# Optimization experiments

Measured on AMD Instinct MI355X. Metric: run time of the kernel, lower is better.

## Reference

```python
import jax, jax.numpy as jnp
import numpy as np

B, NODES, D, DEG = 256, 124, 32, 16
N = B * NODES
EP = NODES * DEG
E = B * EP
L, H, C = 3, 4, 32
NCLS = 40
TMP = 124 + 32 * 2 * L
EPS = 1e-5
NEG_SLOPE = 0.2


def setup_inputs() -> dict:
    key = jax.random.key(0)
    ks = jax.random.split(key, 16)
    x = jax.random.normal(ks[0], (N, D), dtype=jnp.float32)
    # per-graph random edges, guaranteed no self-loops
    src = jax.random.randint(ks[1], (B, EP), 0, NODES)
    off = jax.random.randint(ks[2], (B, EP), 1, NODES)
    dst = (src + off) % NODES
    goff = (jnp.arange(B) * NODES)[:, None]
    edge_index = jnp.stack([(src + goff).reshape(-1), (dst + goff).reshape(-1)]).astype(jnp.int32)
    batch = jnp.repeat(jnp.arange(B), NODES).astype(jnp.int32)
    conv_W = jax.random.normal(ks[3], (L, D, H * C), dtype=jnp.float32) / np.sqrt(D)
    conv_att_l = jax.random.normal(ks[4], (L, H, C), dtype=jnp.float32) * 0.1
    conv_att_r = jax.random.normal(ks[5], (L, H, C), dtype=jnp.float32) * 0.1
    conv_bias = jnp.zeros((L, C), dtype=jnp.float32)
    bn_gamma = jnp.ones((L, C), dtype=jnp.float32)
    bn_beta = jnp.zeros((L, C), dtype=jnp.float32)
    lin1_W = jax.random.normal(ks[6], (NODES * C, 124), dtype=jnp.float32) / np.sqrt(NODES * C)
    lin1_b = jnp.zeros((124,), dtype=jnp.float32)
    bn1_gamma = jnp.ones((124,), dtype=jnp.float32)
    bn1_beta = jnp.zeros((124,), dtype=jnp.float32)
    lin2_W = jax.random.normal(ks[7], (TMP, NCLS), dtype=jnp.float32) / np.sqrt(TMP)
    lin2_b = jnp.zeros((NCLS,), dtype=jnp.float32)
    return dict(x=x, edge_index=edge_index, batch=batch, conv_W=conv_W,
                conv_att_l=conv_att_l, conv_att_r=conv_att_r, conv_bias=conv_bias,
                bn_gamma=bn_gamma, bn_beta=bn_beta, lin1_W=lin1_W, lin1_b=lin1_b,
                bn1_gamma=bn1_gamma, bn1_beta=bn1_beta, lin2_W=lin2_W, lin2_b=lin2_b)


def _supergat_mx(x, src, dst, W, att_l, att_r, bias):
    # SuperGATConv, attention_type='MX', concat=False (mean over heads), eval mode
    h = (x @ W).reshape(N, H, C)              # [N,H,C]
    x_j = h[src]                              # source / message features [E',H,C]
    x_i = h[dst]                              # target features
    logits = jnp.sum(x_i * x_j, -1)           # [E',H] dot-product logits
    alpha = jnp.sum(x_j * att_l, -1) + jnp.sum(x_i * att_r, -1)
    alpha = alpha * jax.nn.sigmoid(logits)
    alpha = jax.nn.leaky_relu(alpha, NEG_SLOPE)
    # scatter-softmax over incoming edges of each target node
    amax = jax.ops.segment_max(alpha, dst, num_segments=N)
    ex = jnp.exp(alpha - amax[dst])
    denom = jax.ops.segment_sum(ex, dst, num_segments=N)
    a = ex / (denom[dst] + 1e-16)             # [E',H]
    out = jax.ops.segment_sum(x_j * a[..., None], dst, num_segments=N)  # [N,H,C]
    return out.mean(axis=1) + bias            # concat=False -> head mean, [N,C]


def _batchnorm(x, gamma, beta):
    mu = x.mean(0)
    var = x.var(0)
    return (x - mu) * jax.lax.rsqrt(var + EPS) * gamma + beta


def reference(x, edge_index, batch, conv_W, conv_att_l, conv_att_r, conv_bias,
              bn_gamma, bn_beta, lin1_W, lin1_b, bn1_gamma, bn1_beta, lin2_W, lin2_b):
    # add self loops once (input edges contain none)
    sl = jnp.arange(N, dtype=edge_index.dtype)
    src = jnp.concatenate([edge_index[0], sl])
    dst = jnp.concatenate([edge_index[1], sl])
    inter = []
    for l in range(L):
        x = _supergat_mx(x, src, dst, conv_W[l], conv_att_l[l], conv_att_r[l], conv_bias[l])
        x = _batchnorm(x, bn_gamma[l], bn_beta[l])
        x = jax.nn.relu(x)
        cnt = jax.ops.segment_sum(jnp.ones((N,), x.dtype), batch, num_segments=B)
        gmean = jax.ops.segment_sum(x, batch, num_segments=B) / cnt[:, None]
        gmax = jax.ops.segment_max(x, batch, num_segments=B)
        inter.append(jnp.concatenate([gmean, gmax], 1))   # [B, 2C]
    x = x.reshape(B, NODES * C)
    x = x @ lin1_W + lin1_b
    x = _batchnorm(x, bn1_gamma, bn1_beta)
    x = jnp.concatenate([x] + inter, 1)                   # inter_connect=True
    x = jax.nn.relu(x)
    return x @ lin2_W + lin2_b                            # [B, NCLS]
```

## Files before the change

### kernel.cpp

```cpp
#include <hip/hip_runtime.h>
#include <math.h>

#define NN 31744
#define NE 507904
#define EP 1984
#define NODES 124
#define NB 256
#define CC 32
#define HC 128
#define FEAT_DIM 316
#define NCLS 40
#define NC 3968
#define EXCAP 192

typedef __attribute__((ext_vector_type(8))) short bf16x8;
typedef __attribute__((ext_vector_type(4))) float f32x4;

#define LOG2E  1.44269504f
#define LOG2E5 0.28853901f

__device__ __forceinline__ unsigned short f2bf(float f) {
    unsigned u = __float_as_uint(f);
    u = u + 0x7FFFu + ((u >> 16) & 1u);
    return (unsigned short)(u >> 16);
}
__device__ __forceinline__ float bf2f(unsigned short s) {
    return __uint_as_float(((unsigned)s) << 16);
}

__global__ __launch_bounds__(256) void prep_k(const int* __restrict__ ei,
                                              unsigned* __restrict__ gmask,
                                              int* __restrict__ gdst,
                                              int* __restrict__ gdent,
                                              float* __restrict__ bnacc,
                                              const float* __restrict__ W1,
                                              unsigned short* __restrict__ WT) {
    int t = threadIdx.x;
    if (blockIdx.x >= NB) {
        __shared__ float tile[32][33];
        int bb = blockIdx.x - NB;
        int kb = bb >> 2, jb = bb & 3;
        int tr = t >> 5, tc = t & 31;
        for (int r = tr; r < 32; r += 8) {
            int k = kb * 32 + r, j = jb * 32 + tc;
            tile[r][tc] = (j < 124) ? W1[k * 124 + j] : 0.f;
        }
        __syncthreads();
        for (int r = tr; r < 32; r += 8) {
            int j = jb * 32 + r, k = kb * 32 + tc;
            WT[(size_t)j * NC + k] = f2bf(tile[tc][r]);
        }
        return;
    }
    __shared__ unsigned mcnt[NODES * NODES];
    __shared__ int cnt[128], pref[128];
    __shared__ int locs[124][8];
    int g = blockIdx.x;
    if (g == 0 && t < 192) bnacc[t] = 0.f;
    for (int i = t; i < NODES * NODES; i += 256) mcnt[i] = 0u;
    __syncthreads();
    for (int e = t; e < EP; e += 256) {
        int s = ei[g * EP + e] - g * NODES;
        int d = ei[NE + g * EP + e] - g * NODES;
        atomicAdd(&mcnt[d * NODES + s], 1u);
    }
    __syncthreads();
    int nd = 0;
    if (t < 124) {
        unsigned m[4] = {0u, 0u, 0u, 0u};
        for (int s = 0; s < NODES; ++s) {
            unsigned c = mcnt[t * NODES + s] + (s == t ? 1u : 0u);
            if (c) {
                m[s >> 5] |= 1u << (s & 31);
                if (c > 1u && nd < 8) { locs[t][nd] = (s << 8) | (int)c; nd++; }
            }
        }
        uint4 mm; mm.x = m[0]; mm.y = m[1]; mm.z = m[2]; mm.w = m[3];
        *(uint4*)&gmask[(size_t)(g * NODES + t) * 4] = mm;
        cnt[t] = nd;
    } else if (t < 128) cnt[t] = 0;
    __syncthreads();
    if (t < 128) pref[t] = cnt[t];
    __syncthreads();
    for (int off = 1; off < 128; off <<= 1) {
        int v = (t >= off && t < 128) ? pref[t - off] : 0;
        __syncthreads();
        if (t < 128) pref[t] += v;
        __syncthreads();
    }
    if (t < 124) {
        int off = pref[t] - cnt[t];
        gdst[g * 132 + t] = off < EXCAP ? off : EXCAP;
        for (int j = 0; j < nd; ++j)
            if (off + j < EXCAP) gdent[g * EXCAP + off + j] = locs[t][j];
    }
    if (t == 0) {
        int tot = pref[127];
        gdst[g * 132 + 124] = tot < EXCAP ? tot : EXCAP;
    }
}

#define HS 136
#define TS 136
#define XS 40
#define ABS 136
#define PWS 40

__global__ __launch_bounds__(1024, 1) void conv_graph(
    const float* __restrict__ xin, const float* __restrict__ W,
    const float* __restrict__ attl, const float* __restrict__ attr,
    const float* __restrict__ bias,
    const unsigned* __restrict__ gmask, const int* __restrict__ gdst,
    const int* __restrict__ gdent,
    const float* __restrict__ bnprev, const float* __restrict__ gprev,
    const float* __restrict__ bprev, float* __restrict__ feat, int lprev,
    float* __restrict__ y, float* __restrict__ bnacc) {

    __shared__ short hbh[128 * HS];
    __shared__ short hbl[128 * HS];
    __shared__ short hTall[128 * TS];
    __shared__ short pwbuf[16 * 1280];
    __shared__ short attBuf[16 * ABS];
    __shared__ float ALs[4][128], ARs[4][128];
    __shared__ unsigned mask[128][4];
    __shared__ unsigned short dupst[136];
    __shared__ unsigned dupent[EXCAP];
    __shared__ float bias_s[32];
    __shared__ float bsum[8][32], bsq[8][32];
    __shared__ float pmean[32];
    __shared__ int pmax[32];

    int g = blockIdx.x, t = threadIdx.x, base = g * NODES;
    short* xh  = pwbuf;
    short* xl  = pwbuf + 5120;
    short* WTh = hTall;
    short* WTl = hTall + 5120;

    if (t < 32) { pmean[t] = 0.f; pmax[t] = 0; }
    __syncthreads();

    {
        const float4* xsrc = (const float4*)(xin + (size_t)base * CC);
        for (int i = t; i < 992; i += 1024) {
            float4 v = xsrc[i];
            int n = i >> 3, c4 = i & 7;
            if (lprev >= 0) {
                float vv[4] = {v.x, v.y, v.z, v.w};
#pragma unroll
                for (int q = 0; q < 4; ++q) {
                    int c = c4 * 4 + q;
                    float mu = bnprev[c] * (1.f / NN);
                    float var = bnprev[32 + c] * (1.f / NN) - mu * mu;
                    float sc = rsqrtf(var + 1e-5f) * gprev[c];
                    float xv = (vv[q] - mu) * sc + bprev[c];
                    xv = fmaxf(xv, 0.f);
                    vv[q] = xv;
                    atomicAdd(&pmean[c], xv);
                    atomicMax(&pmax[c], __float_as_int(xv));
                }
                v.x = vv[0]; v.y = vv[1]; v.z = vv[2]; v.w = vv[3];
            }
            unsigned short h0 = f2bf(v.x), h1 = f2bf(v.y), h2 = f2bf(v.z), h3 = f2bf(v.w);
            unsigned short l0 = f2bf(v.x - bf2f(h0)), l1 = f2bf(v.y - bf2f(h1));
            unsigned short l2 = f2bf(v.z - bf2f(h2)), l3 = f2bf(v.w - bf2f(h3));
            uint2 ph; ph.x = ((unsigned)h1 << 16) | h0; ph.y = ((unsigned)h3 << 16) | h2;
            uint2 pl; pl.x = ((unsigned)l1 << 16) | l0; pl.y = ((unsigned)l3 << 16) | l2;
            *(uint2*)&xh[n * XS + c4 * 4] = ph;
            *(uint2*)&xl[n * XS + c4 * 4] = pl;
        }
        if (t < 4 * XS) { xh[124 * XS + t] = 0; xl[124 * XS + t] = 0; }
    }
    {
        int hc = t & 127, mq = t >> 7, ks = mq * 4;
        unsigned short hh4[4], ll4[4];
#pragma unroll
        for (int q = 0; q < 4; ++q) {
            float w = W[(ks + q) * HC + hc];
            hh4[q] = f2bf(w);
            ll4[q] = f2bf(w - bf2f(hh4[q]));
        }
        uint2 ph; ph.x = ((unsigned)hh4[1] << 16) | hh4[0]; ph.y = ((unsigned)hh4[3] << 16) | hh4[2];
        uint2 pl; pl.x = ((unsigned)ll4[1] << 16) | ll4[0]; pl.y = ((unsigned)ll4[3] << 16) | ll4[2];
        *(uint2*)&WTh[hc * XS + ks] = ph;
        *(uint2*)&WTl[hc * XS + ks] = pl;
    }
    for (int i = t; i < 2048; i += 1024) {
        int n = i >> 7, k = i & 127;
        float v = 0.f;
        int hidx = n & 3;
        if (n < 8 && (k >> 5) == hidx)
            v = (n < 4) ? attl[hidx * 32 + (k & 31)] : attr[hidx * 32 + (k & 31)];
        attBuf[n * ABS + k] = (short)f2bf(v);
    }
    if (t < CC) bias_s[t] = bias[t];
    if (t < 128) {
        if (t < 124) {
            uint4 m = *(const uint4*)&gmask[(size_t)(base + t) * 4];
            mask[t][0] = m.x; mask[t][1] = m.y; mask[t][2] = m.z; mask[t][3] = m.w;
        } else { mask[t][0] = 0u; mask[t][1] = 0u; mask[t][2] = 0u; mask[t][3] = 0u; }
    }
    if (t < 136) dupst[t] = (unsigned short)gdst[g * 132 + (t < 124 ? t : 124)];
    if (t >= 832 && t < 832 + EXCAP) dupent[t - 832] = (unsigned)gdent[g * EXCAP + (t - 832)];
    __syncthreads();

    if (lprev >= 0 && t < 32) {
        float* fp = feat + g * FEAT_DIM + NODES + lprev * 64;
        fp[t] = pmean[t] * (1.f / NODES);
        fp[32 + t] = __int_as_float(pmax[t]);
    }

    int wv = t >> 6, l = t & 63;
    int l15 = l & 15, l4 = l >> 4;

#pragma unroll
    for (int j = 0; j < 4; ++j) {
        int idx = wv * 4 + j;
        int tr = idx >> 3, tc = idx & 7;
        bf16x8 ah = *(bf16x8*)&xh[(tr * 16 + l15) * XS + l4 * 8];
        bf16x8 al_ = *(bf16x8*)&xl[(tr * 16 + l15) * XS + l4 * 8];
        bf16x8 bh = *(bf16x8*)&WTh[(tc * 16 + l15) * XS + l4 * 8];
        bf16x8 bl_ = *(bf16x8*)&WTl[(tc * 16 + l15) * XS + l4 * 8];
        f32x4 z = {0.f, 0.f, 0.f, 0.f};
        f32x4 c0 = __builtin_amdgcn_mfma_f32_16x16x32_bf16(ah, bh, z, 0, 0, 0);
        f32x4 c1 = __builtin_amdgcn_mfma_f32_16x16x32_bf16(ah, bl_, z, 0, 0, 0);
        f32x4 c2 = __builtin_amdgcn_mfma_f32_16x16x32_bf16(al_, bh, z, 0, 0, 0);
        f32x4 c = (c0 + c1) + c2;
        int hc = tc * 16 + l15;
#pragma unroll
        for (int r = 0; r < 4; ++r) {
            int n = tr * 16 + l4 * 4 + r;
            float s = c[r];
            unsigned short hi = f2bf(s);
            hbh[n * HS + hc] = (short)hi;
            hbl[n * HS + hc] = (short)f2bf(s - bf2f(hi));
        }
    }
    __syncthreads();

    if (wv < 8) {
        f32x4 c = {0.f, 0.f, 0.f, 0.f};
#pragma unroll
        for (int kb = 0; kb < 4; ++kb) {
            bf16x8 a = *(bf16x8*)&hbh[(wv * 16 + l15) * HS + kb * 32 + l4 * 8];
            bf16x8 b = *(bf16x8*)&attBuf[l15 * ABS + kb * 32 + l4 * 8];
            c = __builtin_amdgcn_mfma_f32_16x16x32_bf16(a, b, c, 0, 0, 0);
        }
        if (l15 < 8) {
#pragma unroll
            for (int r = 0; r < 4; ++r) {
                int n = wv * 16 + l4 * 4 + r;
                if (l15 < 4) ALs[l15][n] = c[r];
                else         ARs[l15 - 4][n] = c[r];
            }
        }
    }
#pragma unroll
    for (int hh2 = 0; hh2 < 4; ++hh2) {
        int k = t & 31, n4 = t >> 5;
        unsigned short r4[4];
#pragma unroll
        for (int r = 0; r < 4; ++r)
            r4[r] = (unsigned short)hbh[(n4 * 4 + r) * HS + hh2 * 32 + k];
        uint2 pk;
        pk.x = ((unsigned)r4[1] << 16) | r4[0];
        pk.y = ((unsigned)r4[3] << 16) | r4[2];
        *(uint2*)&hTall[(hh2 * 32 + k) * TS + n4 * 4] = pk;
    }
    __syncthreads();

    int DJ = wv >> 1;
    float accA[4] = {0.f, 0.f, 0.f, 0.f};
    float accB[4] = {0.f, 0.f, 0.f, 0.f};
    {
        int hh0 = (wv & 1) * 2;
        short* pwb = pwbuf + wv * 1280;
        int dst = DJ * 16 + l15;
        uint4 mrow = *(uint4*)&mask[dst][0];
        unsigned mwords[4] = {mrow.x, mrow.y, mrow.z, mrow.w};
        unsigned cntp[8];
#pragma unroll
        for (int SI = 0; SI < 8; ++SI) {
            unsigned mw = (mwords[SI >> 1] >> ((SI & 1) * 16 + l4 * 4)) & 0xFu;
            cntp[SI] = (mw & 1u) | ((mw & 2u) << 7) | ((mw & 4u) << 14) | ((mw & 8u) << 21);
        }
        {
            int s0 = dupst[dst], s1 = dupst[dst + 1];
            for (int e = s0; e < s1; ++e) {
                unsigned ent = dupent[e];
                unsigned src = (ent >> 8) & 255u;
                unsigned SI = src >> 4;
                unsigned r = (src & 15u) - (unsigned)(l4 * 4);
                if (r < 4u) {
                    unsigned sh = 8u * r;
                    cntp[SI] = (cntp[SI] & ~(255u << sh)) | ((ent & 255u) << sh);
                }
            }
        }

#define GRAM(kb, slot) { \
    _Pragma("unroll") \
    for (int s2 = 0; s2 < 2; ++s2) { \
        int SI = (kb) * 2 + s2; \
        int ao = (SI * 16 + l15) * HS + hh * 32 + l4 * 8; \
        bf16x8 ah = *(bf16x8*)&hbh[ao]; \
        bf16x8 al_ = *(bf16x8*)&hbl[ao]; \
        f32x4 z2 = {0.f, 0.f, 0.f, 0.f}; \
        f32x4 c0 = __builtin_amdgcn_mfma_f32_16x16x32_bf16(ah, gb, z2, 0, 0, 0); \
        f32x4 c1 = __builtin_amdgcn_mfma_f32_16x16x32_bf16(ah, gl, z2, 0, 0, 0); \
        f32x4 c2 = __builtin_amdgcn_mfma_f32_16x16x32_bf16(al_, gb, z2, 0, 0, 0); \
        f32x4 c = (c0 + c1) + c2; \
        int src0 = SI * 16 + l4 * 4; \
        float4 al4 = *(float4*)&ALs[hh][src0]; \
        unsigned cp = cntp[SI]; \
        float pv[4]; \
        _Pragma("unroll") \
        for (int r = 0; r < 4; ++r) { \
            float e2 = __builtin_amdgcn_exp2f(-LOG2E * c[r]); \
            float sig = __builtin_amdgcn_rcpf(1.f + e2); \
            float a2 = (((const float*)&al4)[r] + ar) * sig; \
            float m = fmaxf(a2 * LOG2E, a2 * LOG2E5); \
            float cr = (float)((cp >> (8 * r)) & 255u); \
            pv[r] = __builtin_amdgcn_exp2f(m) * cr; \
        } \
        sden += (pv[0] + pv[1]) + (pv[2] + pv[3]); \
        unsigned w0_, w1_; \
        asm("v_cvt_pk_bf16_f32 %0, %1, %2" : "=v"(w0_) : "v"(pv[0]), "v"(pv[1])); \
        asm("v_cvt_pk_bf16_f32 %0, %1, %2" : "=v"(w1_) : "v"(pv[2]), "v"(pv[3])); \
        uint2 pk_; pk_.x = w0_; pk_.y = w1_; \
        *(uint2*)&pwb[(slot) * 640 + l15 * PWS + s2 * 16 + l4 * 4] = pk_; \
    } }

#define PVOP(kb, slot) { \
    bf16x8 a = *(bf16x8*)&pwb[(slot) * 640 + l15 * PWS + l4 * 8]; \
    bf16x8 b0 = *(bf16x8*)&hTall[(hh * 32 + l15) * TS + (kb) * 32 + l4 * 8]; \
    bf16x8 b1 = *(bf16x8*)&hTall[(hh * 32 + 16 + l15) * TS + (kb) * 32 + l4 * 8]; \
    num0 = __builtin_amdgcn_mfma_f32_16x16x32_bf16(a, b0, num0, 0, 0, 0); \
    num1 = __builtin_amdgcn_mfma_f32_16x16x32_bf16(a, b1, num1, 0, 0, 0); }

#pragma unroll
        for (int jj = 0; jj < 2; ++jj) {
            int hh = hh0 + jj;
            bf16x8 gb = *(bf16x8*)&hbh[dst * HS + hh * 32 + l4 * 8];
            bf16x8 gl = *(bf16x8*)&hbl[dst * HS + hh * 32 + l4 * 8];
            float ar = ARs[hh][dst];
            float sden = 0.f;
            f32x4 num0 = {0.f, 0.f, 0.f, 0.f};
            f32x4 num1 = {0.f, 0.f, 0.f, 0.f};
            GRAM(0, 0);
            GRAM(1, 1); PVOP(0, 0);
            GRAM(2, 0); PVOP(1, 1);
            GRAM(3, 1); PVOP(2, 0);
            PVOP(3, 1);
            sden += __shfl_xor(sden, 16, 64);
            sden += __shfl_xor(sden, 32, 64);
#pragma unroll
            for (int r = 0; r < 4; ++r) {
                float dn = __shfl(sden, l4 * 4 + r, 64) + 1e-16f;
                accA[r] += ((float*)&num0)[r] / dn;
                accB[r] += ((float*)&num1)[r] / dn;
            }
        }
#undef GRAM
#undef PVOP
    }
    __syncthreads();

    float* exch = (float*)pwbuf;
    if (wv & 1) {
#pragma unroll
        for (int r = 0; r < 4; ++r) {
            exch[DJ * 512 + l15 * 16 + l4 * 4 + r] = accA[r];
            exch[DJ * 512 + 256 + l15 * 16 + l4 * 4 + r] = accB[r];
        }
    }
    __syncthreads();

    if (!(wv & 1)) {
        float sA = 0.f, qA = 0.f, sB = 0.f, qB = 0.f;
#pragma unroll
        for (int r = 0; r < 4; ++r) {
            int n = DJ * 16 + l4 * 4 + r;
            float a = accA[r] + exch[DJ * 512 + l15 * 16 + l4 * 4 + r];
            float b = accB[r] + exch[DJ * 512 + 256 + l15 * 16 + l4 * 4 + r];
            a = 0.25f * a + bias_s[l15];
            b = 0.25f * b + bias_s[16 + l15];
            if (n < NODES) {
                y[(size_t)(base + n) * CC + l15] = a;
                y[(size_t)(base + n) * CC + 16 + l15] = b;
                sA += a; qA += a * a; sB += b; qB += b * b;
            }
        }
        sA += __shfl_xor(sA, 16, 64); sA += __shfl_xor(sA, 32, 64);
        qA += __shfl_xor(qA, 16, 64); qA += __shfl_xor(qA, 32, 64);
        sB += __shfl_xor(sB, 16, 64); sB += __shfl_xor(sB, 32, 64);
        qB += __shfl_xor(qB, 16, 64); qB += __shfl_xor(qB, 32, 64);
        if (l < 16) {
            bsum[DJ][l15] = sA; bsum[DJ][16 + l15] = sB;
            bsq[DJ][l15] = qA;  bsq[DJ][16 + l15] = qB;
        }
    }
    __syncthreads();
    if (t < CC) {
        float S = 0.f, Q = 0.f;
#pragma unroll
        for (int w = 0; w < 8; ++w) { S += bsum[w][t]; Q += bsq[w][t]; }
        atomicAdd(&bnacc[t], S);
        atomicAdd(&bnacc[CC + t], Q);
    }
}

__global__ void bn_relu_pool(const float* __restrict__ y, const float* __restrict__ acc,
                             const float* __restrict__ gamma, const float* __restrict__ beta,
                             unsigned short* __restrict__ xbf, float* __restrict__ feat, int l) {
    int g = blockIdx.x;
    int t = threadIdx.x;
    int c = t & 31, r0 = t >> 5;
    float mu = acc[c] * (1.f / NN);
    float var = acc[32 + c] * (1.f / NN) - mu * mu;
    float sc = rsqrtf(var + 1e-5f) * gamma[c];
    float bt = beta[c];
    float s = 0.f, mx = -INFINITY;
    for (int r = r0; r < NODES; r += 4) {
        int i = (g * NODES + r) * CC + c;
        float v = (y[i] - mu) * sc + bt;
        v = fmaxf(v, 0.f);
        xbf[i] = f2bf(v);
        s += v; mx = fmaxf(mx, v);
    }
    __shared__ float ls[128], lm[128];
    ls[t] = s; lm[t] = mx;
    __syncthreads();
    if (t < 32) {
        float S = ls[t] + ls[32 + t] + ls[64 + t] + ls[96 + t];
        float M = fmaxf(fmaxf(lm[t], lm[32 + t]), fmaxf(lm[64 + t], lm[96 + t]));
        float* fp = feat + g * FEAT_DIM + NODES + l * 64;
        fp[t] = S * (1.f / NODES);
        fp[32 + t] = M;
    }
}

#define L1_KS 4
#define L1_KC 992
#define XP 1000
__global__ __launch_bounds__(512) void lin1_mfma(const unsigned short* __restrict__ Xb,
                                                 const unsigned short* __restrict__ WT,
                                                 float* __restrict__ part) {
    __shared__ unsigned short Xs[16 * XP];
    int mt = blockIdx.x >> 2, kp = blockIdx.x & 3;
    int t = threadIdx.x;
    int wv = t >> 6, l = t & 63, l15 = l & 15, l4 = l >> 4;
    int M0 = mt * 16, k0 = kp * L1_KC;
    for (int i = t; i < 16 * 124; i += 512) {
        int r = i / 124, c = i - r * 124;
        *(uint4*)&Xs[r * XP + c * 8] = *(const uint4*)&Xb[(size_t)(M0 + r) * NC + k0 + c * 8];
    }
    __syncthreads();
    int N0 = wv * 16;
    f32x4 acc = {0.f, 0.f, 0.f, 0.f};
#pragma unroll 4
    for (int kk = 0; kk < 31; ++kk) {
        bf16x8 a = *(bf16x8*)&Xs[l15 * XP + kk * 32 + l4 * 8];
        bf16x8 b = *(const bf16x8*)&WT[(size_t)(N0 + l15) * NC + k0 + kk * 32 + l4 * 8];
        acc = __builtin_amdgcn_mfma_f32_16x16x32_bf16(a, b, acc, 0, 0, 0);
    }
    if (N0 + l15 < 124) {
#pragma unroll
        for (int r = 0; r < 4; ++r)
            part[(size_t)kp * NB * 124 + (M0 + l4 * 4 + r) * 124 + N0 + l15] = acc[r];
    }
}

__global__ __launch_bounds__(512) void bn1_fused(const float* __restrict__ part,
                                                 const float* __restrict__ b,
                                                 const float* __restrict__ gamma,
                                                 const float* __restrict__ beta,
                                                 float* __restrict__ out1,
                                                 float* __restrict__ feat) {
    __shared__ float ps[4][124], pq[4][124], smu[124], ssc[124], sbt[124];
    int t = threadIdx.x;
    int c = t & 127, seg = t >> 7;
    float s = 0.f, q = 0.f;
    if (c < 124) {
        float bb = b[c];
        for (int r = seg * 64; r < seg * 64 + 64; ++r) {
            int i = r * 124 + c;
            float v = bb + part[i] + part[NB * 124 + i]
                    + part[2 * NB * 124 + i] + part[3 * NB * 124 + i];
            out1[i] = v;
            s += v; q += v * v;
        }
        ps[seg][c] = s; pq[seg][c] = q;
    }
    __syncthreads();
    if (t < 124) {
        float S = ps[0][t] + ps[1][t] + ps[2][t] + ps[3][t];
        float Q = pq[0][t] + pq[1][t] + pq[2][t] + pq[3][t];
        float mu = S * (1.f / NB);
        float var = Q * (1.f / NB) - mu * mu;
        smu[t] = mu; ssc[t] = rsqrtf(var + 1e-5f) * gamma[t]; sbt[t] = beta[t];
    }
    __syncthreads();
    if (c < 124) {
        for (int r = seg * 64; r < seg * 64 + 64; ++r) {
            float v = (out1[r * 124 + c] - smu[c]) * ssc[c] + sbt[c];
            feat[r * FEAT_DIM + c] = fmaxf(v, 0.f);
        }
    }
}

__global__ void lin2_k(const float* __restrict__ feat, const float* __restrict__ W,
                       const float* __restrict__ b, float* __restrict__ out) {
    __shared__ float psum[8][40];
    int g = blockIdx.x;
    int t = threadIdx.x;
    int j = t % 40, u = t / 40;
    if (u < 8) {
        int k0 = u * 40, k1 = (u == 7) ? FEAT_DIM : k0 + 40;
        float s = 0.f;
        for (int k = k0; k < k1; ++k) s += feat[g * FEAT_DIM + k] * W[k * NCLS + j];
        psum[u][j] = s;
    }
    __syncthreads();
    if (t < NCLS) {
        float s = b[t];
#pragma unroll
        for (int u2 = 0; u2 < 8; ++u2) s += psum[u2][t];
        out[g * NCLS + t] = s;
    }
}

extern "C" void kernel_launch(void* const* d_in, const int* in_sizes, int n_in,
                              void* d_out, int out_size, void* d_ws, size_t ws_size,
                              hipStream_t stream) {
    const float* x      = (const float*)d_in[0];
    const int*   ei     = (const int*)d_in[1];
    const float* conv_W = (const float*)d_in[3];
    const float* att_l  = (const float*)d_in[4];
    const float* att_r  = (const float*)d_in[5];
    const float* conv_b = (const float*)d_in[6];
    const float* bn_g   = (const float*)d_in[7];
    const float* bn_b   = (const float*)d_in[8];
    const float* lin1_W = (const float*)d_in[9];
    const float* lin1_b = (const float*)d_in[10];
    const float* bn1_g  = (const float*)d_in[11];
    const float* bn1_b  = (const float*)d_in[12];
    const float* lin2_W = (const float*)d_in[13];
    const float* lin2_b = (const float*)d_in[14];

    float* ws = (float*)d_ws;
    float* y = ws;
    unsigned short* xbf = (unsigned short*)(y + (size_t)NN * CC);
    float* bnacc = (float*)(xbf + (size_t)NN * CC);
    float* feat  = bnacc + 192;
    float* out1  = feat + NB * FEAT_DIM;
    float* part  = out1 + NB * 124;
    unsigned short* WT = (unsigned short*)(part + L1_KS * NB * 124);
    unsigned* gmask = (unsigned*)(WT + (size_t)128 * NC);
    int* gdst  = (int*)(gmask + (size_t)NN * 4);
    int* gdent = gdst + NB * 132;

    prep_k<<<NB + (NC / 32) * 4, 256, 0, stream>>>(ei, gmask, gdst, gdent, bnacc,
                                                   lin1_W, WT);

    const float* xin = x;
    for (int l = 0; l < 3; ++l) {
        const float* bnprev = (l == 0) ? nullptr : bnacc + (l - 1) * 64;
        const float* gprev  = (l == 0) ? bn_g : bn_g + (l - 1) * CC;
        const float* bprev  = (l == 0) ? bn_b : bn_b + (l - 1) * CC;
        conv_graph<<<NB, 1024, 0, stream>>>(xin, conv_W + l * CC * HC,
                                            att_l + l * HC, att_r + l * HC,
                                            conv_b + l * CC, gmask, gdst, gdent,
                                            bnprev, gprev, bprev, feat, l - 1,
                                            y, bnacc + l * 64);
        xin = y;
    }

    bn_relu_pool<<<NB, 128, 0, stream>>>(y, bnacc + 128, bn_g + 2 * CC, bn_b + 2 * CC,
                                         xbf, feat, 2);
    lin1_mfma<<<64, 512, 0, stream>>>(xbf, WT, part);
    bn1_fused<<<1, 512, 0, stream>>>(part, lin1_b, bn1_g, bn1_b, out1, feat);
    lin2_k<<<NB, 320, 0, stream>>>(feat, lin2_W, lin2_b, (float*)d_out);
}
```

Baseline: 151.3 us.

## Fuse graph adjacency build into first conv and final BN/pool into lin1

The per-graph edge-count/mask/duplicate-list construction moves from prep_k into the first conv_graph launch, which builds it in shared memory and also writes it to global for later layers; prep_k now only transposes lin1 weights and zeroes accumulators and feature slots. The separate bn_relu_pool kernel is removed: lin1_mfma reads fp32 conv output, applies the last batchnorm+ReLU while staging its bf16 tile, and accumulates mean/max pooling into feat with atomics. This drops a launch and the bf16 intermediate round-trip, but adds serial adjacency work to the first conv's critical path and atomic pooling in lin1.

```diff
diff --git a/kernel.cpp b/kernel.cpp
--- a/kernel.cpp
+++ b/kernel.cpp
@@ -28,75 +28,29 @@
     return __uint_as_float(((unsigned)s) << 16);
 }
 
-__global__ __launch_bounds__(256) void prep_k(const int* __restrict__ ei,
-                                              unsigned* __restrict__ gmask,
-                                              int* __restrict__ gdst,
-                                              int* __restrict__ gdent,
+__global__ __launch_bounds__(256) void prep_k(const float* __restrict__ W1,
+                                              unsigned short* __restrict__ WT,
                                               float* __restrict__ bnacc,
-                                              const float* __restrict__ W1,
-                                              unsigned short* __restrict__ WT) {
+                                              float* __restrict__ feat) {
     int t = threadIdx.x;
-    if (blockIdx.x >= NB) {
-        __shared__ float tile[32][33];
-        int bb = blockIdx.x - NB;
-        int kb = bb >> 2, jb = bb & 3;
-        int tr = t >> 5, tc = t & 31;
-        for (int r = tr; r < 32; r += 8) {
-            int k = kb * 32 + r, j = jb * 32 + tc;
-            tile[r][tc] = (j < 124) ? W1[k * 124 + j] : 0.f;
-        }
-        __syncthreads();
-        for (int r = tr; r < 32; r += 8) {
-            int j = jb * 32 + r, k = kb * 32 + tc;
-            WT[(size_t)j * NC + k] = f2bf(tile[tc][r]);
-        }
+    if (blockIdx.x >= 496) {
+        int idx = (blockIdx.x - 496) * 256 + t;
+        int g2 = idx >> 6, slot = idx & 63;
+        feat[g2 * FEAT_DIM + 252 + slot] = 0.f;
         return;
     }
-    __shared__ unsigned mcnt[NODES * NODES];
-    __shared__ int cnt[128], pref[128];
-    __shared__ int locs[124][8];
-    int g = blockIdx.x;
-    if (g == 0 && t < 192) bnacc[t] = 0.f;
-    for (int i = t; i < NODES * NODES; i += 256) mcnt[i] = 0u;
-    __syncthreads();
-    for (int e = t; e < EP; e += 256) {
-        int s = ei[g * EP + e] - g * NODES;
-        int d = ei[NE + g * EP + e] - g * NODES;
-        atomicAdd(&mcnt[d * NODES + s], 1u);
-    }
-    __syncthreads();
-    int nd = 0;
-    if (t < 124) {
-        unsigned m[4] = {0u, 0u, 0u, 0u};
-        for (int s = 0; s < NODES; ++s) {
-            unsigned c = mcnt[t * NODES + s] + (s == t ? 1u : 0u);
-            if (c) {
-                m[s >> 5] |= 1u << (s & 31);
-                if (c > 1u && nd < 8) { locs[t][nd] = (s << 8) | (int)c; nd++; }
-            }
-        }
-        uint4 mm; mm.x = m[0]; mm.y = m[1]; mm.z = m[2]; mm.w = m[3];
-        *(uint4*)&gmask[(size_t)(g * NODES + t) * 4] = mm;
-        cnt[t] = nd;
-    } else if (t < 128) cnt[t] = 0;
-    __syncthreads();
-    if (t < 128) pref[t] = cnt[t];
-    __syncthreads();
-    for (int off = 1; off < 128; off <<= 1) {
-        int v = (t >= off && t < 128) ? pref[t - off] : 0;
-        __syncthreads();
-        if (t < 128) pref[t] += v;
-        __syncthreads();
-    }
-    if (t < 124) {
-        int off = pref[t] - cnt[t];
-        gdst[g * 132 + t] = off < EXCAP ? off : EXCAP;
-        for (int j = 0; j < nd; ++j)
-            if (off + j < EXCAP) gdent[g * EXCAP + off + j] = locs[t][j];
-    }
-    if (t == 0) {
-        int tot = pref[127];
-        gdst[g * 132 + 124] = tot < EXCAP ? tot : EXCAP;
+    __shared__ float tile[32][33];
+    if (blockIdx.x == 0 && t < 192) bnacc[t] = 0.f;
+    int kb = blockIdx.x >> 2, jb = blockIdx.x & 3;
+    int tr = t >> 5, tc = t & 31;
+    for (int r = tr; r < 32; r += 8) {
+        int k = kb * 32 + r, j = jb * 32 + tc;
+        tile[r][tc] = (j < 124) ? W1[k * 124 + j] : 0.f;
+    }
+    __syncthreads();
+    for (int r = tr; r < 32; r += 8) {
+        int j = jb * 32 + r, k = kb * 32 + tc;
+        WT[(size_t)j * NC + k] = f2bf(tile[tc][r]);
     }
 }
 
@@ -110,14 +64,13 @@
     const float* __restrict__ xin, const float* __restrict__ W,
     const float* __restrict__ attl, const float* __restrict__ attr,
     const float* __restrict__ bias,
-    const unsigned* __restrict__ gmask, const int* __restrict__ gdst,
-    const int* __restrict__ gdent,
+    unsigned* __restrict__ gmask, int* __restrict__ gdst, int* __restrict__ gdent,
+    const int* __restrict__ ei,
     const float* __restrict__ bnprev, const float* __restrict__ gprev,
     const float* __restrict__ bprev, float* __restrict__ feat, int lprev,
     float* __restrict__ y, float* __restrict__ bnacc) {
 
-    __shared__ short hbh[128 * HS];
-    __shared__ short hbl[128 * HS];
+    __shared__ short hpool[2 * 128 * HS];
     __shared__ short hTall[128 * TS];
     __shared__ short pwbuf[16 * 1280];
     __shared__ short attBuf[16 * ABS];
@@ -129,7 +82,10 @@
     __shared__ float bsum[8][32], bsq[8][32];
     __shared__ float pmean[32];
     __shared__ int pmax[32];
-
+    __shared__ int cnt_s[128], pref_s[128];
+
+    short* hbh = hpool;
+    short* hbl = hpool + 128 * HS;
     int g = blockIdx.x, t = threadIdx.x, base = g * NODES;
     short* xh  = pwbuf;
     short* xl  = pwbuf + 5120;
@@ -170,20 +126,6 @@
         }
         if (t < 4 * XS) { xh[124 * XS + t] = 0; xl[124 * XS + t] = 0; }
     }
-    {
-        int hc = t & 127, mq = t >> 7, ks = mq * 4;
-        unsigned short hh4[4], ll4[4];
-#pragma unroll
-        for (int q = 0; q < 4; ++q) {
-            float w = W[(ks + q) * HC + hc];
-            hh4[q] = f2bf(w);
-            ll4[q] = f2bf(w - bf2f(hh4[q]));
-        }
-        uint2 ph; ph.x = ((unsigned)hh4[1] << 16) | hh4[0]; ph.y = ((unsigned)hh4[3] << 16) | hh4[2];
-        uint2 pl; pl.x = ((unsigned)ll4[1] << 16) | ll4[0]; pl.y = ((unsigned)ll4[3] << 16) | ll4[2];
-        *(uint2*)&WTh[hc * XS + ks] = ph;
-        *(uint2*)&WTl[hc * XS + ks] = pl;
-    }
     for (int i = t; i < 2048; i += 1024) {
         int n = i >> 7, k = i & 127;
         float v = 0.f;
@@ -193,21 +135,94 @@
         attBuf[n * ABS + k] = (short)f2bf(v);
     }
     if (t < CC) bias_s[t] = bias[t];
-    if (t < 128) {
+
+    if (lprev < 0) {
+        unsigned* mcnt = (unsigned*)hpool;
+        int (*locs)[8] = (int(*)[8])hTall;
+        for (int i = t; i < NODES * NODES; i += 1024) mcnt[i] = 0u;
+        __syncthreads();
+        for (int e = t; e < EP; e += 1024) {
+            int s = ei[g * EP + e] - base;
+            int d = ei[NE + g * EP + e] - base;
+            atomicAdd(&mcnt[d * NODES + s], 1u);
+        }
+        __syncthreads();
+        int nd = 0;
         if (t < 124) {
-            uint4 m = *(const uint4*)&gmask[(size_t)(base + t) * 4];
-            mask[t][0] = m.x; mask[t][1] = m.y; mask[t][2] = m.z; mask[t][3] = m.w;
-        } else { mask[t][0] = 0u; mask[t][1] = 0u; mask[t][2] = 0u; mask[t][3] = 0u; }
-    }
-    if (t < 136) dupst[t] = (unsigned short)gdst[g * 132 + (t < 124 ? t : 124)];
-    if (t >= 832 && t < 832 + EXCAP) dupent[t - 832] = (unsigned)gdent[g * EXCAP + (t - 832)];
-    __syncthreads();
-
+            unsigned m[4] = {0u, 0u, 0u, 0u};
+            for (int s = 0; s < NODES; ++s) {
+                unsigned c = mcnt[t * NODES + s] + (s == t ? 1u : 0u);
+                if (c) {
+                    m[s >> 5] |= 1u << (s & 31);
+                    if (c > 1u && nd < 8) { locs[t][nd] = (s << 8) | (int)c; nd++; }
+                }
+            }
+            mask[t][0] = m[0]; mask[t][1] = m[1]; mask[t][2] = m[2]; mask[t][3] = m[3];
+            uint4 mm; mm.x = m[0]; mm.y = m[1]; mm.z = m[2]; mm.w = m[3];
+            *(uint4*)&gmask[(size_t)(base + t) * 4] = mm;
+            cnt_s[t] = nd;
+        } else if (t < 128) {
+            cnt_s[t] = 0;
+            mask[t][0] = 0u; mask[t][1] = 0u; mask[t][2] = 0u; mask[t][3] = 0u;
+        }
+        __syncthreads();
+        if (t < 128) pref_s[t] = cnt_s[t];
+        __syncthreads();
+        for (int off = 1; off < 128; off <<= 1) {
+            int v = (t >= off && t < 128) ? pref_s[t - off] : 0;
+            __syncthreads();
+            if (t < 128) pref_s[t] += v;
+            __syncthreads();
+        }
+        if (t < 124) {
+            int off = pref_s[t] - cnt_s[t];
+            int offc = off < EXCAP ? off : EXCAP;
+            dupst[t] = (unsigned short)offc;
+            gdst[g * 132 + t] = offc;
+            for (int j = 0; j < nd; ++j)
+                if (off + j < EXCAP) {
+                    dupent[off + j] = (unsigned)locs[t][j];
+                    gdent[g * EXCAP + off + j] = locs[t][j];
+                }
+        } else if (t < 136) {
+            int tot = pref_s[127];
+            int totc = tot < EXCAP ? tot : EXCAP;
+            dupst[t] = (unsigned short)totc;
+            if (t == 124) gdst[g * 132 + 124] = totc;
+        }
+        __syncthreads();
+    } else {
+        if (t < 128) {
+            if (t < 124) {
+                uint4 m = *(const uint4*)&gmask[(size_t)(base + t) * 4];
+                mask[t][0] = m.x; mask[t][1] = m.y; mask[t][2] = m.z; mask[t][3] = m.w;
+            } else { mask[t][0] = 0u; mask[t][1] = 0u; mask[t][2] = 0u; mask[t][3] = 0u; }
+        }
+        if (t < 136) dupst[t] = (unsigned short)gdst[g * 132 + (t < 124 ? t : 124)];
+        if (t >= 832 && t < 832 + EXCAP) dupent[t - 832] = (unsigned)gdent[g * EXCAP + (t - 832)];
+        __syncthreads();
+    }
+
+    {
+        int hc = t & 127, mq = t >> 7, ks = mq * 4;
+        unsigned short hh4[4], ll4[4];
+#pragma unroll
+        for (int q = 0; q < 4; ++q) {
+            float w = W[(ks + q) * HC + hc];
+            hh4[q] = f2bf(w);
+            ll4[q] = f2bf(w - bf2f(hh4[q]));
+        }
+        uint2 ph; ph.x = ((unsigned)hh4[1] << 16) | hh4[0]; ph.y = ((unsigned)hh4[3] << 16) | hh4[2];
+        uint2 pl; pl.x = ((unsigned)ll4[1] << 16) | ll4[0]; pl.y = ((unsigned)ll4[3] << 16) | ll4[2];
+        *(uint2*)&WTh[hc * XS + ks] = ph;
+        *(uint2*)&WTl[hc * XS + ks] = pl;
+    }
     if (lprev >= 0 && t < 32) {
         float* fp = feat + g * FEAT_DIM + NODES + lprev * 64;
         fp[t] = pmean[t] * (1.f / NODES);
         fp[32 + t] = __int_as_float(pmax[t]);
     }
+    __syncthreads();
 
     int wv = t >> 6, l = t & 63;
     int l15 = l & 15, l4 = l >> 4;
@@ -409,52 +424,59 @@
     }
 }
 
-__global__ void bn_relu_pool(const float* __restrict__ y, const float* __restrict__ acc,
-                             const float* __restrict__ gamma, const float* __restrict__ beta,
-                             unsigned short* __restrict__ xbf, float* __restrict__ feat, int l) {
-    int g = blockIdx.x;
-    int t = threadIdx.x;
-    int c = t & 31, r0 = t >> 5;
-    float mu = acc[c] * (1.f / NN);
-    float var = acc[32 + c] * (1.f / NN) - mu * mu;
-    float sc = rsqrtf(var + 1e-5f) * gamma[c];
-    float bt = beta[c];
-    float s = 0.f, mx = -INFINITY;
-    for (int r = r0; r < NODES; r += 4) {
-        int i = (g * NODES + r) * CC + c;
-        float v = (y[i] - mu) * sc + bt;
-        v = fmaxf(v, 0.f);
-        xbf[i] = f2bf(v);
-        s += v; mx = fmaxf(mx, v);
-    }
-    __shared__ float ls[128], lm[128];
-    ls[t] = s; lm[t] = mx;
-    __syncthreads();
-    if (t < 32) {
-        float S = ls[t] + ls[32 + t] + ls[64 + t] + ls[96 + t];
-        float M = fmaxf(fmaxf(lm[t], lm[32 + t]), fmaxf(lm[64 + t], lm[96 + t]));
-        float* fp = feat + g * FEAT_DIM + NODES + l * 64;
-        fp[t] = S * (1.f / NODES);
-        fp[32 + t] = M;
-    }
-}
-
 #define L1_KS 4
 #define L1_KC 992
 #define XP 1000
-__global__ __launch_bounds__(512) void lin1_mfma(const unsigned short* __restrict__ Xb,
+__global__ __launch_bounds__(512) void lin1_mfma(const float* __restrict__ Y,
+                                                 const float* __restrict__ bnacc,
+                                                 const float* __restrict__ bng,
+                                                 const float* __restrict__ bnb,
                                                  const unsigned short* __restrict__ WT,
-                                                 float* __restrict__ part) {
+                                                 float* __restrict__ part,
+                                                 float* __restrict__ feat) {
     __shared__ unsigned short Xs[16 * XP];
+    __shared__ float smu[32], ssc[32], sbt[32];
     int mt = blockIdx.x >> 2, kp = blockIdx.x & 3;
     int t = threadIdx.x;
+    if (t < 32) {
+        float mu = bnacc[128 + t] * (1.f / NN);
+        float var = bnacc[160 + t] * (1.f / NN) - mu * mu;
+        smu[t] = mu;
+        ssc[t] = rsqrtf(var + 1e-5f) * bng[2 * CC + t];
+        sbt[t] = bnb[2 * CC + t];
+    }
+    __syncthreads();
+    int M0 = mt * 16, k0 = kp * L1_KC;
+    for (int i = t; i < 16 * 248; i += 512) {
+        int r = i / 248, c4 = i - r * 248;
+        float4 v = *(const float4*)&Y[(size_t)(M0 + r) * NC + k0 + c4 * 4];
+        int cb = (c4 * 4) & 31;
+        float vv[4] = {v.x, v.y, v.z, v.w};
+        unsigned short hb[4];
+#pragma unroll
+        for (int q = 0; q < 4; ++q) {
+            int c = cb + q;
+            float xv = fmaxf((vv[q] - smu[c]) * ssc[c] + sbt[c], 0.f);
+            hb[q] = f2bf(xv);
+        }
+        uint2 pk;
+        pk.x = ((unsigned)hb[1] << 16) | hb[0];
+        pk.y = ((unsigned)hb[3] << 16) | hb[2];
+        *(uint2*)&Xs[r * XP + c4 * 4] = pk;
+    }
+    __syncthreads();
+    {
+        int gl = t >> 5, ch = t & 31;
+        float s = 0.f, mx = 0.f;
+        for (int nd2 = 0; nd2 < 31; ++nd2) {
+            float v = bf2f(Xs[gl * XP + nd2 * 32 + ch]);
+            s += v; mx = fmaxf(mx, v);
+        }
+        float* fp = feat + (size_t)(M0 + gl) * FEAT_DIM + 252;
+        atomicAdd(&fp[ch], s * (1.f / NODES));
+        atomicMax((int*)&fp[32 + ch], __float_as_int(mx));
+    }
     int wv = t >> 6, l = t & 63, l15 = l & 15, l4 = l >> 4;
-    int M0 = mt * 16, k0 = kp * L1_KC;
-    for (int i = t; i < 16 * 124; i += 512) {
-        int r = i / 124, c = i - r * 124;
-        *(uint4*)&Xs[r * XP + c * 8] = *(const uint4*)&Xb[(size_t)(M0 + r) * NC + k0 + c * 8];
-    }
-    __syncthreads();
     int N0 = wv * 16;
     f32x4 acc = {0.f, 0.f, 0.f, 0.f};
 #pragma unroll 4
@@ -549,8 +571,7 @@
 
     float* ws = (float*)d_ws;
     float* y = ws;
-    unsigned short* xbf = (unsigned short*)(y + (size_t)NN * CC);
-    float* bnacc = (float*)(xbf + (size_t)NN * CC);
+    float* bnacc = y + (size_t)NN * CC;
     float* feat  = bnacc + 192;
     float* out1  = feat + NB * FEAT_DIM;
     float* part  = out1 + NB * 124;
@@ -559,8 +580,7 @@
     int* gdst  = (int*)(gmask + (size_t)NN * 4);
     int* gdent = gdst + NB * 132;
 
-    prep_k<<<NB + (NC / 32) * 4, 256, 0, stream>>>(ei, gmask, gdst, gdent, bnacc,
-                                                   lin1_W, WT);
+    prep_k<<<560, 256, 0, stream>>>(lin1_W, WT, bnacc, feat);
 
     const float* xin = x;
     for (int l = 0; l < 3; ++l) {
@@ -569,15 +589,13 @@
         const float* bprev  = (l == 0) ? bn_b : bn_b + (l - 1) * CC;
         conv_graph<<<NB, 1024, 0, stream>>>(xin, conv_W + l * CC * HC,
                                             att_l + l * HC, att_r + l * HC,
-                                            conv_b + l * CC, gmask, gdst, gdent,
+                                            conv_b + l * CC, gmask, gdst, gdent, ei,
                                             bnprev, gprev, bprev, feat, l - 1,
                                             y, bnacc + l * 64);
         xin = y;
     }
 
-    bn_relu_pool<<<NB, 128, 0, stream>>>(y, bnacc + 128, bn_g + 2 * CC, bn_b + 2 * CC,
-                                         xbf, feat, 2);
-    lin1_mfma<<<64, 512, 0, stream>>>(xbf, WT, part);
+    lin1_mfma<<<64, 512, 0, stream>>>(y, bnacc, bn_g, bn_b, WT, part, feat);
     bn1_fused<<<1, 512, 0, stream>>>(part, lin1_b, bn1_g, bn1_b, out1, feat);
     lin2_k<<<NB, 320, 0, stream>>>(feat, lin2_W, lin2_b, (float*)d_out);
 }
```

Measured after the change: 152.0 us. No clear change (+0.4%).
